# Optimization experiments

Hardware: AMD Instinct MI355X
Metric: run time of the kernel (lower is better)

Reference implementation:

```python
import jax, jax.numpy as jnp
import numpy as np
from jax import lax


def conv3d(x, w, b):
    # x: (B,W,D,H,Cin), w: (kW,kD,kH,Cin,Cout), 'same' padding, stride 1
    return lax.conv_general_dilated(
        x, w, window_strides=(1, 1, 1), padding='SAME',
        dimension_numbers=('NDHWC', 'DHWIO', 'NDHWC')) + b


def proj(x, w, b, s, o):
    # Conv3D -> BatchNorm (inference, folded to per-channel affine) -> ReLU
    return jax.nn.relu(conv3d(x, w, b) * s + o)


def setup_inputs() -> dict:
    key = jax.random.key(0)
    ks = jax.random.split(key, 6)
    B, W, D, H, C = 2, 16, 16, 16, 32
    WS = 0.05  # weight scale to keep sigmoid of the NxN chain unsaturated
    return {
        'x': jax.random.normal(ks[0], (B, W, D, H, C), jnp.float32),
        'gamma': jax.random.uniform(ks[1], (1,), jnp.float32),
        'q_w': jax.random.normal(ks[2], (1, 3, 1, C, 8), jnp.float32) * WS,
        'q_b': jnp.zeros((8,), jnp.float32),
        'q_s': jnp.ones((8,), jnp.float32),
        'q_o': jnp.zeros((8,), jnp.float32),
        'k_w': jax.random.normal(ks[3], (3, 1, 1, C, 8), jnp.float32) * WS,
        'k_b': jnp.zeros((8,), jnp.float32),
        'k_s': jnp.ones((8,), jnp.float32),
        'k_o': jnp.zeros((8,), jnp.float32),
        'j_w': jax.random.normal(ks[4], (1, 1, 3, C, 8), jnp.float32) * WS,
        'j_b': jnp.zeros((8,), jnp.float32),
        'j_s': jnp.ones((8,), jnp.float32),
        'j_o': jnp.zeros((8,), jnp.float32),
        'v_w': jax.random.normal(ks[5], (1, 1, 1, C, C), jnp.float32) * WS,
        'v_b': jnp.zeros((C,), jnp.float32),
        'v_s': jnp.ones((C,), jnp.float32),
        'v_o': jnp.zeros((C,), jnp.float32),
    }


def reference(x, gamma, q_w, q_b, q_s, q_o, k_w, k_b, k_s, k_o,
              j_w, j_b, j_s, j_o, v_w, v_b, v_s, v_o):
    B, W, D, H, C = x.shape
    N = W * D * H
    # Q/K/J: (B,W,D,H,8) -> row-major reshape to (B,8,N) exactly as tf Reshape
    Qt = jnp.swapaxes(proj(x, q_w, q_b, q_s, q_o).reshape(B, -1, N), 1, 2)  # (B,N,8)
    K = proj(x, k_w, k_b, k_s, k_o).reshape(B, -1, N)                        # (B,8,N)
    Jt = jnp.swapaxes(proj(x, j_w, j_b, j_s, j_o).reshape(B, -1, N), 1, 2)  # (B,N,8)
    V = proj(x, v_w, v_b, v_s, v_o).reshape(B, N, -1)                        # (B,N,C)
    m1 = jnp.matmul(Qt, K)          # (B,N,N)
    m2 = jnp.matmul(Jt, K)          # (B,N,N)
    affinity = jax.nn.sigmoid(jnp.matmul(m1, m2))  # (B,N,N)
    weights = jnp.matmul(affinity, V).reshape(B, W, D, H, C)
    return gamma * weights + x
```

## Files before the change

### kernel.cpp

```cpp
#include <hip/hip_runtime.h>
#include <cstddef>

#define NN 4096

typedef short bf16x8 __attribute__((ext_vector_type(8)));
typedef float f32x4 __attribute__((ext_vector_type(4)));
typedef float f32x2 __attribute__((ext_vector_type(2)));

__device__ __forceinline__ unsigned short f2bf(float f) {
    union { float f; unsigned u; } v; v.f = f;
    unsigned r = v.u + 0x7fffu + ((v.u >> 16) & 1u);
    return (unsigned short)(r >> 16);
}

__global__ __launch_bounds__(256) void kA(
    const float* __restrict__ x,
    const float* __restrict__ qw, const float* __restrict__ qb,
    const float* __restrict__ qs, const float* __restrict__ qo,
    const float* __restrict__ kw, const float* __restrict__ kb,
    const float* __restrict__ ks, const float* __restrict__ ko,
    const float* __restrict__ jw, const float* __restrict__ jb,
    const float* __restrict__ js, const float* __restrict__ jo,
    const float* __restrict__ vw, const float* __restrict__ vb,
    const float* __restrict__ vs, const float* __restrict__ vo,
    float* __restrict__ Qf, float* __restrict__ Kf,
    unsigned short* __restrict__ Vt, float* __restrict__ Mm)
{
    __shared__ float vw_s[1024];
    __shared__ float cw_s[3 * 776];
    __shared__ float Kl[32][8];
    __shared__ float Jl[32][8];
    const int t = threadIdx.x;
    for (int i = t; i < 1024; i += 256) vw_s[i] = vw[i];
    for (int i = t; i < 768; i += 256) {
        cw_s[i]        = qw[i];
        cw_s[776 + i]  = kw[i];
        cw_s[1552 + i] = jw[i];
    }
    __syncthreads();

    const int spi = t >> 3;
    const int gsp = blockIdx.x * 32 + spi;
    const int b   = gsp >> 12;
    const int sp  = gsp & 4095;
    const int w = sp >> 8, d = (sp >> 4) & 15, h = sp & 15;
    const float4* xr = (const float4*)(x + (size_t)gsp * 32);

    {
        const int c4 = t & 7;
        float4 acc = make_float4(0.f, 0.f, 0.f, 0.f);
        #pragma unroll
        for (int c8 = 0; c8 < 8; ++c8) {
            const float4 xv = xr[c8];
            #pragma unroll
            for (int k = 0; k < 4; ++k) {
                const float xs = (k == 0) ? xv.x : (k == 1) ? xv.y : (k == 2) ? xv.z : xv.w;
                const float4 wv = *(const float4*)&vw_s[(c8 * 4 + k) * 32 + c4 * 4];
                acc.x += xs * wv.x; acc.y += xs * wv.y;
                acc.z += xs * wv.z; acc.w += xs * wv.w;
            }
        }
        const float4 bb = ((const float4*)vb)[c4];
        const float4 sc = ((const float4*)vs)[c4];
        const float4 oo = ((const float4*)vo)[c4];
        float4 r;
        r.x = fmaxf((acc.x + bb.x) * sc.x + oo.x, 0.f);
        r.y = fmaxf((acc.y + bb.y) * sc.y + oo.y, 0.f);
        r.z = fmaxf((acc.z + bb.z) * sc.z + oo.z, 0.f);
        r.w = fmaxf((acc.w + bb.w) * sc.w + oo.w, 0.f);
        unsigned short* vt = Vt + (size_t)b * 131072 + (size_t)(c4 * 4) * 4096 + sp;
        vt[0]        = f2bf(r.x);
        vt[4096]     = f2bf(r.y);
        vt[2 * 4096] = f2bf(r.z);
        vt[3 * 4096] = f2bf(r.w);
    }

    {
        const int g = t & 7;
        if (g < 6) {
            const int conv = g >> 1;
            const int co4  = g & 1;
            const int coord  = (conv == 0) ? d : (conv == 1) ? w : h;
            const int stride = (conv == 0) ? 16 : (conv == 1) ? 256 : 1;
            const float* cw = cw_s + conv * 776;
            float4 acc = make_float4(0.f, 0.f, 0.f, 0.f);
            #pragma unroll
            for (int tap = 0; tap < 3; ++tap) {
                const int cc = coord + tap - 1;
                if (cc < 0 || cc > 15) continue;
                const float4* xt = (const float4*)(x + (size_t)(gsp + (tap - 1) * stride) * 32);
                #pragma unroll
                for (int c8 = 0; c8 < 8; ++c8) {
                    const float4 xv = xt[c8];
                    #pragma unroll
                    for (int k = 0; k < 4; ++k) {
                        const float xs = (k == 0) ? xv.x : (k == 1) ? xv.y : (k == 2) ? xv.z : xv.w;
                        const float4 wv = *(const float4*)&cw[tap * 256 + (c8 * 4 + k) * 8 + co4 * 4];
                        acc.x += xs * wv.x; acc.y += xs * wv.y;
                        acc.z += xs * wv.z; acc.w += xs * wv.w;
                    }
                }
            }
            const float* bbp = (conv == 0) ? qb : (conv == 1) ? kb : jb;
            const float* scp = (conv == 0) ? qs : (conv == 1) ? ks : js;
            const float* oop = (conv == 0) ? qo : (conv == 1) ? ko : jo;
            const float4 bb = ((const float4*)bbp)[co4];
            const float4 sc = ((const float4*)scp)[co4];
            const float4 oo = ((const float4*)oop)[co4];
            float4 r;
            r.x = fmaxf((acc.x + bb.x) * sc.x + oo.x, 0.f);
            r.y = fmaxf((acc.y + bb.y) * sc.y + oo.y, 0.f);
            r.z = fmaxf((acc.z + bb.z) * sc.z + oo.z, 0.f);
            r.w = fmaxf((acc.w + bb.w) * sc.w + oo.w, 0.f);
            if (conv == 0) {
                ((float4*)(Qf + (size_t)b * 32768 + (size_t)sp * 8))[co4] = r;
            } else if (conv == 1) {
                ((float4*)(Kf + (size_t)b * 32768 + (size_t)sp * 8))[co4] = r;
                *(float4*)&Kl[spi][co4 * 4] = r;
            } else {
                *(float4*)&Jl[spi][co4 * 4] = r;
            }
        }
    }

    __syncthreads();
    if (t < 64) {
        const int r = t >> 3, s = t & 7;
        float acc = 0.f;
        #pragma unroll 8
        for (int i = 0; i < 32; ++i) acc += Kl[i][r] * Jl[i][s];
        atomicAdd(&Mm[b * 64 + t], acc);
    }
}

__global__ __launch_bounds__(256) void kD(
    const float* __restrict__ Qf, const float* __restrict__ Mm,
    const float* __restrict__ Kf, const unsigned short* __restrict__ Vt,
    const float* __restrict__ gamma, float* __restrict__ out)
{
    const int blk = blockIdx.x;
    const int jsp = blk & 7;
    const int rt  = (blk >> 3) & 63;
    const int b   = blk >> 9;
    const int i0  = rt * 64;
    const int j0  = jsp * 512;
    const int t   = threadIdx.x;
    const int jg = t & 15, rg = t >> 4;
    const int w = t >> 6, lane = t & 63;
    const int m = lane & 15, quad = lane >> 4;

    __shared__ float m_s[64];
    __shared__ float kt_s[8][516];
    __shared__ unsigned short s_lds[2][64][72];

    const float* Kb = Kf + (size_t)b * 32768;
    const unsigned short* Vb = Vt + (size_t)b * 131072;

    if (t < 64) m_s[t] = Mm[b * 64 + t];
    #pragma unroll
    for (int v = 0; v < 4; ++v) {
        const int idx = t + v * 256;
        const int r = idx >> 7, j4 = (idx & 127) << 2;
        *(float4*)&kt_s[r][j4] = *(const float4*)(Kb + (size_t)r * 4096 + j0 + j4);
    }
    __syncthreads();

    float P2[4][8];
    {
        float a[4][8];
        #pragma unroll
        for (int r = 0; r < 8; ++r) {
            const float* qr = Qf + (size_t)b * 32768 + (size_t)r * 4096 + i0 + rg * 4;
            #pragma unroll
            for (int ri = 0; ri < 4; ++ri) a[ri][r] = qr[ri];
        }
        #pragma unroll
        for (int s = 0; s < 8; ++s) {
            #pragma unroll
            for (int ri = 0; ri < 4; ++ri) {
                float acc = 0.f;
                #pragma unroll
                for (int r = 0; r < 8; ++r) acc += a[ri][r] * m_s[r * 8 + s];
                P2[ri][s] = acc * -1.44269504f;
            }
        }
    }

    f32x4 acc0 = {0.f, 0.f, 0.f, 0.f};
    f32x4 acc1 = {0.f, 0.f, 0.f, 0.f};

    #pragma unroll 1
    for (int jc = 0; jc < 8; ++jc) {
        const int jb = j0 + jc * 64;
        const bf16x8 bv00 = *(const bf16x8*)(Vb + (size_t)m * 4096 + jb + quad * 8);
        const bf16x8 bv10 = *(const bf16x8*)(Vb + (size_t)m * 4096 + jb + 32 + quad * 8);
        const bf16x8 bv01 = *(const bf16x8*)(Vb + (size_t)(16 + m) * 4096 + jb + quad * 8);
        const bf16x8 bv11 = *(const bf16x8*)(Vb + (size_t)(16 + m) * 4096 + jb + 32 + quad * 8);

        unsigned short (*sl)[72] = s_lds[jc & 1];

        unsigned hpk[4][2];
        #pragma unroll
        for (int tp = 0; tp < 2; ++tp) {
            const int jcol = jg * 4 + tp * 2;
            f32x2 pa[4];
            #pragma unroll
            for (int ri = 0; ri < 4; ++ri) pa[ri] = (f32x2){0.f, 0.f};
            #pragma unroll
            for (int r = 0; r < 8; ++r) {
                const f32x2 kv = *(const f32x2*)&kt_s[r][jcol];
                #pragma unroll
                for (int ri = 0; ri < 4; ++ri)
                    pa[ri] = __builtin_elementwise_fma((f32x2){P2[ri][r], P2[ri][r]}, kv, pa[ri]);
            }
            #pragma unroll
            for (int ri = 0; ri < 4; ++ri) {
                float e0, e1;
                asm("v_exp_f32 %0, %1" : "=v"(e0) : "v"(pa[ri].x));
                asm("v_exp_f32 %0, %1" : "=v"(e1) : "v"(pa[ri].y));
                const float s0 = __builtin_amdgcn_rcpf(1.0f + e0);
                const float s1 = __builtin_amdgcn_rcpf(1.0f + e1);
                unsigned pk;
                asm("v_cvt_pk_bf16_f32 %0, %1, %2" : "=v"(pk) : "v"(s0), "v"(s1));
                hpk[ri][tp] = pk;
            }
        }
        #pragma unroll
        for (int ri = 0; ri < 4; ++ri)
            *(uint2*)&sl[rg * 4 + ri][jg * 4] = make_uint2(hpk[ri][0], hpk[ri][1]);

        __syncthreads();

        __builtin_amdgcn_s_setprio(1);
        const bf16x8 af0 = *(const bf16x8*)&sl[w * 16 + m][quad * 8];
        const bf16x8 af1 = *(const bf16x8*)&sl[w * 16 + m][32 + quad * 8];
        acc0 = __builtin_amdgcn_mfma_f32_16x16x32_bf16(af0, bv00, acc0, 0, 0, 0);
        acc1 = __builtin_amdgcn_mfma_f32_16x16x32_bf16(af0, bv01, acc1, 0, 0, 0);
        acc0 = __builtin_amdgcn_mfma_f32_16x16x32_bf16(af1, bv10, acc0, 0, 0, 0);
        acc1 = __builtin_amdgcn_mfma_f32_16x16x32_bf16(af1, bv11, acc1, 0, 0, 0);
        __builtin_amdgcn_s_setprio(0);
    }

    const float g = gamma[0];
    #pragma unroll
    for (int reg = 0; reg < 4; ++reg) {
        const int row = i0 + w * 16 + quad * 4 + reg;
        float* op = out + ((size_t)b * 4096 + row) * 32 + m;
        atomicAdd(op,      g * acc0[reg]);
        atomicAdd(op + 16, g * acc1[reg]);
    }
}

extern "C" void kernel_launch(void* const* d_in, const int* in_sizes, int n_in,
                              void* d_out, int out_size, void* d_ws, size_t ws_size,
                              hipStream_t stream)
{
    const float* x     = (const float*)d_in[0];
    const float* gamma = (const float*)d_in[1];
    const float* qw = (const float*)d_in[2];
    const float* qb = (const float*)d_in[3];
    const float* qs = (const float*)d_in[4];
    const float* qo = (const float*)d_in[5];
    const float* kw = (const float*)d_in[6];
    const float* kb = (const float*)d_in[7];
    const float* ks = (const float*)d_in[8];
    const float* ko = (const float*)d_in[9];
    const float* jw = (const float*)d_in[10];
    const float* jb = (const float*)d_in[11];
    const float* js = (const float*)d_in[12];
    const float* jo = (const float*)d_in[13];
    const float* vw = (const float*)d_in[14];
    const float* vb = (const float*)d_in[15];
    const float* vs = (const float*)d_in[16];
    const float* vo = (const float*)d_in[17];

    float* ws = (float*)d_ws;
    float* Qf = ws;
    float* Kf = ws + 65536;
    float* Mm = ws + 131072;
    unsigned short* Vt = (unsigned short*)(ws + 131200);

    hipMemsetAsync(Mm, 0, 128 * sizeof(float), stream);
    hipMemcpyAsync(d_out, x, (size_t)262144 * sizeof(float),
                   hipMemcpyDeviceToDevice, stream);
    kA<<<256, 256, 0, stream>>>(x, qw, qb, qs, qo, kw, kb, ks, ko,
                                jw, jb, js, jo, vw, vb, vs, vo,
                                Qf, Kf, Vt, Mm);
    kD<<<1024, 256, 0, stream>>>(Qf, Mm, Kf, Vt, gamma, (float*)d_out);
}
```

Measured before the change: 121.6 us.

## Restructure projection kernel, split K·J reduction, fold residual copy and gamma

The projection kernel now assigns one thread per output channel over 8 spatial points per block (1024 blocks instead of 256). It reuses loaded x rows for the center tap and writes the residual x into out directly, which replaces the device-to-device memcpy. The K^T·J 8x8 reduction moves to a separate small kernel reading a new Jf buffer, so the many per-block atomics are replaced with 16 blocks. Gamma is folded into V before bf16 conversion, and the attention kernel vectorizes Q loads and the sigmoid logits to 4-wide. This adds a third launch and an extra global round-trip for J.

```diff
diff --git a/kernel.cpp b/kernel.cpp
--- a/kernel.cpp
+++ b/kernel.cpp
@@ -1,11 +1,9 @@
 #include <hip/hip_runtime.h>
 #include <cstddef>
 
-#define NN 4096
 
 typedef short bf16x8 __attribute__((ext_vector_type(8)));
 typedef float f32x4 __attribute__((ext_vector_type(4)));
-typedef float f32x2 __attribute__((ext_vector_type(2)));
 
 __device__ __forceinline__ unsigned short f2bf(float f) {
     union { float f; unsigned u; } v; v.f = f;
@@ -23,13 +21,12 @@
     const float* __restrict__ js, const float* __restrict__ jo,
     const float* __restrict__ vw, const float* __restrict__ vb,
     const float* __restrict__ vs, const float* __restrict__ vo,
-    float* __restrict__ Qf, float* __restrict__ Kf,
-    unsigned short* __restrict__ Vt, float* __restrict__ Mm)
+    const float* __restrict__ gamma,
+    float* __restrict__ Qf, float* __restrict__ Kf, float* __restrict__ Jf,
+    unsigned short* __restrict__ Vt, float* __restrict__ out)
 {
     __shared__ float vw_s[1024];
     __shared__ float cw_s[3 * 776];
-    __shared__ float Kl[32][8];
-    __shared__ float Jl[32][8];
     const int t = threadIdx.x;
     for (int i = t; i < 1024; i += 256) vw_s[i] = vw[i];
     for (int i = t; i < 768; i += 256) {
@@ -39,104 +36,98 @@
     }
     __syncthreads();
 
-    const int spi = t >> 3;
-    const int gsp = blockIdx.x * 32 + spi;
+    const int spi = t >> 5;
+    const int g   = t & 31;
+    const int gsp = blockIdx.x * 8 + spi;
     const int b   = gsp >> 12;
     const int sp  = gsp & 4095;
     const int w = sp >> 8, d = (sp >> 4) & 15, h = sp & 15;
+    const float gm = gamma[0];
     const float4* xr = (const float4*)(x + (size_t)gsp * 32);
 
+    float4 xv[8];
+    #pragma unroll
+    for (int c8 = 0; c8 < 8; ++c8) xv[c8] = xr[c8];
+
     {
-        const int c4 = t & 7;
-        float4 acc = make_float4(0.f, 0.f, 0.f, 0.f);
+        const float4 mine = xv[g >> 2];
+        const int q = g & 3;
+        const float xe = (q == 0) ? mine.x : (q == 1) ? mine.y : (q == 2) ? mine.z : mine.w;
+        out[(size_t)gsp * 32 + g] = xe;
+    }
+
+    {
+        float a0 = 0.f, a1 = 0.f, a2 = 0.f, a3 = 0.f;
         #pragma unroll
         for (int c8 = 0; c8 < 8; ++c8) {
-            const float4 xv = xr[c8];
-            #pragma unroll
-            for (int k = 0; k < 4; ++k) {
-                const float xs = (k == 0) ? xv.x : (k == 1) ? xv.y : (k == 2) ? xv.z : xv.w;
-                const float4 wv = *(const float4*)&vw_s[(c8 * 4 + k) * 32 + c4 * 4];
-                acc.x += xs * wv.x; acc.y += xs * wv.y;
-                acc.z += xs * wv.z; acc.w += xs * wv.w;
-            }
-        }
-        const float4 bb = ((const float4*)vb)[c4];
-        const float4 sc = ((const float4*)vs)[c4];
-        const float4 oo = ((const float4*)vo)[c4];
-        float4 r;
-        r.x = fmaxf((acc.x + bb.x) * sc.x + oo.x, 0.f);
-        r.y = fmaxf((acc.y + bb.y) * sc.y + oo.y, 0.f);
-        r.z = fmaxf((acc.z + bb.z) * sc.z + oo.z, 0.f);
-        r.w = fmaxf((acc.w + bb.w) * sc.w + oo.w, 0.f);
-        unsigned short* vt = Vt + (size_t)b * 131072 + (size_t)(c4 * 4) * 4096 + sp;
-        vt[0]        = f2bf(r.x);
-        vt[4096]     = f2bf(r.y);
-        vt[2 * 4096] = f2bf(r.z);
-        vt[3 * 4096] = f2bf(r.w);
-    }
-
-    {
-        const int g = t & 7;
-        if (g < 6) {
-            const int conv = g >> 1;
-            const int co4  = g & 1;
-            const int coord  = (conv == 0) ? d : (conv == 1) ? w : h;
-            const int stride = (conv == 0) ? 16 : (conv == 1) ? 256 : 1;
-            const float* cw = cw_s + conv * 776;
-            float4 acc = make_float4(0.f, 0.f, 0.f, 0.f);
-            #pragma unroll
-            for (int tap = 0; tap < 3; ++tap) {
-                const int cc = coord + tap - 1;
-                if (cc < 0 || cc > 15) continue;
-                const float4* xt = (const float4*)(x + (size_t)(gsp + (tap - 1) * stride) * 32);
-                #pragma unroll
-                for (int c8 = 0; c8 < 8; ++c8) {
-                    const float4 xv = xt[c8];
-                    #pragma unroll
-                    for (int k = 0; k < 4; ++k) {
-                        const float xs = (k == 0) ? xv.x : (k == 1) ? xv.y : (k == 2) ? xv.z : xv.w;
-                        const float4 wv = *(const float4*)&cw[tap * 256 + (c8 * 4 + k) * 8 + co4 * 4];
-                        acc.x += xs * wv.x; acc.y += xs * wv.y;
-                        acc.z += xs * wv.z; acc.w += xs * wv.w;
-                    }
-                }
-            }
-            const float* bbp = (conv == 0) ? qb : (conv == 1) ? kb : jb;
-            const float* scp = (conv == 0) ? qs : (conv == 1) ? ks : js;
-            const float* oop = (conv == 0) ? qo : (conv == 1) ? ko : jo;
-            const float4 bb = ((const float4*)bbp)[co4];
-            const float4 sc = ((const float4*)scp)[co4];
-            const float4 oo = ((const float4*)oop)[co4];
-            float4 r;
-            r.x = fmaxf((acc.x + bb.x) * sc.x + oo.x, 0.f);
-            r.y = fmaxf((acc.y + bb.y) * sc.y + oo.y, 0.f);
-            r.z = fmaxf((acc.z + bb.z) * sc.z + oo.z, 0.f);
-            r.w = fmaxf((acc.w + bb.w) * sc.w + oo.w, 0.f);
-            if (conv == 0) {
-                ((float4*)(Qf + (size_t)b * 32768 + (size_t)sp * 8))[co4] = r;
-            } else if (conv == 1) {
-                ((float4*)(Kf + (size_t)b * 32768 + (size_t)sp * 8))[co4] = r;
-                *(float4*)&Kl[spi][co4 * 4] = r;
-            } else {
-                *(float4*)&Jl[spi][co4 * 4] = r;
-            }
-        }
-    }
-
+            const float4 v = xv[c8];
+            a0 += v.x * vw_s[(c8 * 4 + 0) * 32 + g];
+            a1 += v.y * vw_s[(c8 * 4 + 1) * 32 + g];
+            a2 += v.z * vw_s[(c8 * 4 + 2) * 32 + g];
+            a3 += v.w * vw_s[(c8 * 4 + 3) * 32 + g];
+        }
+        const float vv = fmaxf(((a0 + a1) + (a2 + a3) + vb[g]) * vs[g] + vo[g], 0.f) * gm;
+        Vt[(size_t)b * 131072 + (size_t)g * 4096 + sp] = f2bf(vv);
+    }
+
+    if (g < 24) {
+        const int conv = g >> 3;
+        const int co   = g & 7;
+        const int coord  = (conv == 0) ? d : (conv == 1) ? w : h;
+        const int stride = (conv == 0) ? 16 : (conv == 1) ? 256 : 1;
+        const float* cw = cw_s + conv * 776 + co;
+        float b0 = 0.f, b1 = 0.f, b2 = 0.f, b3 = 0.f;
+        #pragma unroll
+        for (int tap = 0; tap < 3; ++tap) {
+            const int cc = coord + tap - 1;
+            if (cc < 0 || cc > 15) continue;
+            const float4* xt = (const float4*)(x + (size_t)(gsp + (tap - 1) * stride) * 32);
+            const float* wt = cw + tap * 256;
+            #pragma unroll
+            for (int c8 = 0; c8 < 8; ++c8) {
+                const float4 v = (tap == 1) ? xv[c8] : xt[c8];
+                b0 += v.x * wt[(c8 * 4 + 0) * 8];
+                b1 += v.y * wt[(c8 * 4 + 1) * 8];
+                b2 += v.z * wt[(c8 * 4 + 2) * 8];
+                b3 += v.w * wt[(c8 * 4 + 3) * 8];
+            }
+        }
+        const float* bbp = (conv == 0) ? qb : (conv == 1) ? kb : jb;
+        const float* scp = (conv == 0) ? qs : (conv == 1) ? ks : js;
+        const float* oop = (conv == 0) ? qo : (conv == 1) ? ko : jo;
+        const float rv = fmaxf(((b0 + b1) + (b2 + b3) + bbp[co]) * scp[co] + oop[co], 0.f);
+        float* dst = (conv == 0) ? Qf : (conv == 1) ? Kf : Jf;
+        dst[(size_t)b * 32768 + (size_t)sp * 8 + co] = rv;
+    }
+}
+
+__global__ __launch_bounds__(256) void kM(
+    const float* __restrict__ Kf, const float* __restrict__ Jf,
+    float* __restrict__ Mm)
+{
+    const int b = blockIdx.x >> 3, o = blockIdx.x & 7;
+    const int t = threadIdx.x;
+    const int rs = t & 63, r = rs >> 3, s = rs & 7, sub = t >> 6;
+    const float4* Kb = (const float4*)(Kf + (size_t)b * 32768 + (size_t)r * 4096 + o * 512 + sub * 128);
+    const float4* Jb = (const float4*)(Jf + (size_t)b * 32768 + (size_t)s * 4096 + o * 512 + sub * 128);
+    float acc = 0.f;
+    #pragma unroll
+    for (int i = 0; i < 32; ++i) {
+        const float4 kv = Kb[i];
+        const float4 jv = Jb[i];
+        acc += kv.x * jv.x + kv.y * jv.y + kv.z * jv.z + kv.w * jv.w;
+    }
+    __shared__ float sm[256];
+    sm[t] = acc;
     __syncthreads();
-    if (t < 64) {
-        const int r = t >> 3, s = t & 7;
-        float acc = 0.f;
-        #pragma unroll 8
-        for (int i = 0; i < 32; ++i) acc += Kl[i][r] * Jl[i][s];
-        atomicAdd(&Mm[b * 64 + t], acc);
-    }
+    if (t < 64)
+        atomicAdd(&Mm[b * 64 + t], sm[t] + sm[t + 64] + sm[t + 128] + sm[t + 192]);
 }
 
 __global__ __launch_bounds__(256) void kD(
     const float* __restrict__ Qf, const float* __restrict__ Mm,
     const float* __restrict__ Kf, const unsigned short* __restrict__ Vt,
-    const float* __restrict__ gamma, float* __restrict__ out)
+    float* __restrict__ out)
 {
     const int blk = blockIdx.x;
     const int jsp = blk & 7;
@@ -170,9 +161,8 @@
         float a[4][8];
         #pragma unroll
         for (int r = 0; r < 8; ++r) {
-            const float* qr = Qf + (size_t)b * 32768 + (size_t)r * 4096 + i0 + rg * 4;
-            #pragma unroll
-            for (int ri = 0; ri < 4; ++ri) a[ri][r] = qr[ri];
+            const float4 qv = *(const float4*)(Qf + (size_t)b * 32768 + (size_t)r * 4096 + i0 + rg * 4);
+            a[0][r] = qv.x; a[1][r] = qv.y; a[2][r] = qv.z; a[3][r] = qv.w;
         }
         #pragma unroll
         for (int s = 0; s < 8; ++s) {
@@ -200,29 +190,38 @@
         unsigned short (*sl)[72] = s_lds[jc & 1];
 
         unsigned hpk[4][2];
-        #pragma unroll
-        for (int tp = 0; tp < 2; ++tp) {
-            const int jcol = jg * 4 + tp * 2;
-            f32x2 pa[4];
-            #pragma unroll
-            for (int ri = 0; ri < 4; ++ri) pa[ri] = (f32x2){0.f, 0.f};
+        {
+            f32x4 pa[4];
+            #pragma unroll
+            for (int ri = 0; ri < 4; ++ri) pa[ri] = (f32x4){0.f, 0.f, 0.f, 0.f};
             #pragma unroll
             for (int r = 0; r < 8; ++r) {
-                const f32x2 kv = *(const f32x2*)&kt_s[r][jcol];
+                const f32x4 kv = *(const f32x4*)&kt_s[r][(jc << 6) + (jg << 2)];
                 #pragma unroll
-                for (int ri = 0; ri < 4; ++ri)
-                    pa[ri] = __builtin_elementwise_fma((f32x2){P2[ri][r], P2[ri][r]}, kv, pa[ri]);
+                for (int ri = 0; ri < 4; ++ri) {
+                    const float p = P2[ri][r];
+                    pa[ri][0] += p * kv[0];
+                    pa[ri][1] += p * kv[1];
+                    pa[ri][2] += p * kv[2];
+                    pa[ri][3] += p * kv[3];
+                }
             }
             #pragma unroll
             for (int ri = 0; ri < 4; ++ri) {
-                float e0, e1;
-                asm("v_exp_f32 %0, %1" : "=v"(e0) : "v"(pa[ri].x));
-                asm("v_exp_f32 %0, %1" : "=v"(e1) : "v"(pa[ri].y));
+                float e0, e1, e2, e3;
+                asm("v_exp_f32 %0, %1" : "=v"(e0) : "v"(pa[ri][0]));
+                asm("v_exp_f32 %0, %1" : "=v"(e1) : "v"(pa[ri][1]));
+                asm("v_exp_f32 %0, %1" : "=v"(e2) : "v"(pa[ri][2]));
+                asm("v_exp_f32 %0, %1" : "=v"(e3) : "v"(pa[ri][3]));
                 const float s0 = __builtin_amdgcn_rcpf(1.0f + e0);
                 const float s1 = __builtin_amdgcn_rcpf(1.0f + e1);
-                unsigned pk;
-                asm("v_cvt_pk_bf16_f32 %0, %1, %2" : "=v"(pk) : "v"(s0), "v"(s1));
-                hpk[ri][tp] = pk;
+                const float s2 = __builtin_amdgcn_rcpf(1.0f + e2);
+                const float s3 = __builtin_amdgcn_rcpf(1.0f + e3);
+                unsigned pk0, pk1;
+                asm("v_cvt_pk_bf16_f32 %0, %1, %2" : "=v"(pk0) : "v"(s0), "v"(s1));
+                asm("v_cvt_pk_bf16_f32 %0, %1, %2" : "=v"(pk1) : "v"(s2), "v"(s3));
+                hpk[ri][0] = pk0;
+                hpk[ri][1] = pk1;
             }
         }
         #pragma unroll
@@ -241,13 +240,12 @@
         __builtin_amdgcn_s_setprio(0);
     }
 
-    const float g = gamma[0];
     #pragma unroll
     for (int reg = 0; reg < 4; ++reg) {
         const int row = i0 + w * 16 + quad * 4 + reg;
         float* op = out + ((size_t)b * 4096 + row) * 32 + m;
-        atomicAdd(op,      g * acc0[reg]);
-        atomicAdd(op + 16, g * acc1[reg]);
+        atomicAdd(op,      acc0[reg]);
+        atomicAdd(op + 16, acc1[reg]);
     }
 }
 
@@ -277,14 +275,14 @@
     float* ws = (float*)d_ws;
     float* Qf = ws;
     float* Kf = ws + 65536;
-    float* Mm = ws + 131072;
-    unsigned short* Vt = (unsigned short*)(ws + 131200);
+    float* Jf = ws + 131072;
+    float* Mm = ws + 196608;
+    unsigned short* Vt = (unsigned short*)(ws + 196736);
 
     hipMemsetAsync(Mm, 0, 128 * sizeof(float), stream);
-    hipMemcpyAsync(d_out, x, (size_t)262144 * sizeof(float),
-                   hipMemcpyDeviceToDevice, stream);
-    kA<<<256, 256, 0, stream>>>(x, qw, qb, qs, qo, kw, kb, ks, ko,
-                                jw, jb, js, jo, vw, vb, vs, vo,
-                                Qf, Kf, Vt, Mm);
-    kD<<<1024, 256, 0, stream>>>(Qf, Mm, Kf, Vt, gamma, (float*)d_out);
-}
+    kA<<<1024, 256, 0, stream>>>(x, qw, qb, qs, qo, kw, kb, ks, ko,
+                                 jw, jb, js, jo, vw, vb, vs, vo, gamma,
+                                 Qf, Kf, Jf, Vt, (float*)d_out);
+    kM<<<16, 256, 0, stream>>>(Kf, Jf, Mm);
+    kD<<<1024, 256, 0, stream>>>(Qf, Mm, Kf, Vt, (float*)d_out);
+}
```

New measurement: 134.5 us. 10.6% more time.
